# Kernel tuning notes

Measured on AMD Instinct MI355X. Metric: run time of the kernel, lower is better.

## Reference

```python
import jax, jax.numpy as jnp
import numpy as np
from jax import lax

IC, OC, K = 512, 512, 3
EPS = 1e-8
BLUR = np.array([1.0, 3.0, 3.0, 1.0], dtype=np.float32)


def setup_inputs() -> dict:
    key = jax.random.key(0)
    k1, k2 = jax.random.split(key)
    x = jax.random.normal(k1, (1, IC, 128, 128), dtype=jnp.float32)
    weight = jax.random.normal(k2, (1, OC, IC, K, K), dtype=jnp.float32)
    return {"x": x, "weight": weight}


def _blur_kernel():
    k1d = BLUR / BLUR.sum()  # normalize before outer product is equiv (sum of outer = 1)
    k2d = np.outer(k1d, k1d)
    k2d = k2d / k2d.sum()
    k2d = k2d * 4.0  # upsample_factor ** 2
    return jnp.asarray(k2d, dtype=jnp.float32)


def reference(x, weight):
    # x: (1, IC, H, W); weight: (1, OC, IC, K, K)
    scale = 1.0 / np.sqrt(IC * K * K)
    w = scale * weight
    # demodulation (batch = 1)
    demod = lax.rsqrt(jnp.sum(w * w, axis=(2, 3, 4)) + EPS)  # (1, OC)
    w = w * demod[:, :, None, None, None]
    w = w[0]  # (OC, IC, K, K)

    # conv_transpose2d(stride=2, padding=0) == conv with lhs_dilation=2,
    # spatial pad K-1, and spatially-flipped kernel.
    wt = jnp.flip(w, axis=(2, 3))  # (OC, IC, K, K)
    out = lax.conv_general_dilated(
        x, wt,
        window_strides=(1, 1),
        padding=[(K - 1, K - 1), (K - 1, K - 1)],
        lhs_dilation=(2, 2),
        dimension_numbers=("NCHW", "OIHW", "NCHW"),
    )  # (1, OC, 2H+1, 2W+1) = (1, 512, 257, 257)

    # Blur: depthwise FIR filter, pad0 = pad1 = 1, kernel 4x4 (upfirdn2d flips kernel)
    bk = jnp.flip(_blur_kernel(), axis=(0, 1))  # (4, 4), symmetric so flip is a no-op
    bkern = jnp.broadcast_to(bk[None, None], (OC, 1, 4, 4))
    out = lax.conv_general_dilated(
        out, bkern,
        window_strides=(1, 1),
        padding=[(1, 1), (1, 1)],
        feature_group_count=OC,
        dimension_numbers=("NCHW", "OIHW", "NCHW"),
    )  # (1, OC, 256, 256)
    return out
```

## Files before the change

### kernel.cpp

```cpp
#include <hip/hip_runtime.h>
#include <hip/hip_bf16.h>

#define ICN 512
#define OCN 512
#define RS    136
#define NROW  17792
#define GUARD 144
#define XROWS 17936

typedef __attribute__((ext_vector_type(8))) short short8;
typedef __attribute__((ext_vector_type(4))) float f32x4;

__device__ __forceinline__ void gload_lds16(const void* g, void* l) {
  __builtin_amdgcn_global_load_lds(
      (const __attribute__((address_space(1))) void*)g,
      (__attribute__((address_space(3))) void*)l, 16, 0, 0);
}

__global__ __launch_bounds__(256) void wprep_k(const float* __restrict__ w,
                                               __hip_bfloat16* __restrict__ AP) {
  constexpr int WIDX[9] = {0, 2, 6, 8, 1, 7, 3, 5, 4};
  const int oc = blockIdx.x;
  const int tid = threadIdx.x, lane = tid & 63, wv = tid >> 6;

  float v[2][9];
  float s = 0.f;
#pragma unroll
  for (int rep = 0; rep < 2; ++rep) {
    const int ic = tid + rep * 256;
    const float* wp = w + ((size_t)oc * ICN + ic) * 9;
#pragma unroll
    for (int j = 0; j < 9; ++j) { v[rep][j] = wp[j]; s += wp[j] * wp[j]; }
  }
#pragma unroll
  for (int o = 32; o > 0; o >>= 1) s += __shfl_down(s, o, 64);
  __shared__ float red[4];
  if (lane == 0) red[wv] = s;
  __syncthreads();
  const float tot = red[0] + red[1] + red[2] + red[3];
  const float scale2 = 1.0f / 4608.0f;
  const float c = sqrtf(scale2) * rsqrtf(scale2 * tot + 1e-8f);

#pragma unroll
  for (int rep = 0; rep < 2; ++rep) {
    const int ic = tid + rep * 256;
#pragma unroll
    for (int tp = 0; tp < 9; ++tp)
      AP[((size_t)tp * OCN + oc) * ICN + ic] = __float2bfloat16(c * v[rep][WIDX[tp]]);
  }
}

__global__ __launch_bounds__(256) void packx2_k(const float* __restrict__ x,
                                                unsigned int* __restrict__ XP32) {
  const int py  = blockIdx.x;
  const int ic0 = blockIdx.y * 64;
  const int tid = threadIdx.x;
  const int yy  = py - 1;
  const bool rowvalid = (unsigned)yy < 128u;

  __shared__ __hip_bfloat16 T[128 * 65];

  if (rowvalid) {
    const float4* xr = (const float4*)(x + (size_t)ic0 * 16384 + (size_t)yy * 128);
#pragma unroll
    for (int rep = 0; rep < 8; ++rep) {
      const int idx = rep * 256 + tid;
      const int x4 = idx & 31, ici = idx >> 5;
      const float4 v = xr[(size_t)ici * 4096 + x4];
      const int xx = x4 * 4;
      T[(xx + 0) * 65 + ici] = __float2bfloat16(v.x);
      T[(xx + 1) * 65 + ici] = __float2bfloat16(v.y);
      T[(xx + 2) * 65 + ici] = __float2bfloat16(v.z);
      T[(xx + 3) * 65 + ici] = __float2bfloat16(v.w);
    }
  }
  __syncthreads();

  const size_t rowbase = (size_t)(GUARD + py * 136) * 256 + (ic0 >> 1);
  for (int rep = 0; rep < 17; ++rep) {
    const int idx = rep * 256 + tid;
    const int px = idx >> 5, j = idx & 31;
    unsigned int uv = 0;
    if (rowvalid && (unsigned)(px - 1) < 128u) {
      union { __hip_bfloat16 h[2]; unsigned int u; } cv;
      cv.h[0] = T[(px - 1) * 65 + 2 * j];
      cv.h[1] = T[(px - 1) * 65 + 2 * j + 1];
      uv = cv.u;
    }
    XP32[rowbase + (size_t)px * 256 + j] = uv;
  }
}

__global__ __launch_bounds__(256) void zguard_k(unsigned int* __restrict__ XP32) {
  const int r = blockIdx.x;
  const int row = (r < 144) ? r : (r + 17680);
  XP32[(size_t)row * 256 + threadIdx.x] = 0;
}

__global__ __launch_bounds__(256) void gemm_k(const __hip_bfloat16* __restrict__ AP,
                                              const __hip_bfloat16* __restrict__ XPT,
                                              __hip_bfloat16* __restrict__ C) {
  constexpr int NTt[4]   = {4, 2, 2, 1};
  constexpr int TPO[4]   = {0, 4, 6, 8};
  constexpr int SHIFT[9] = {0, 1, 136, 137, 0, 136, 0, 1, 0};
  constexpr int AR[4]    = {129, 129, 128, 128};
  constexpr int AC[4]    = {129, 128, 129, 128};

  const int n0 = blockIdx.x * 128, oc0 = blockIdx.y * 128, ph = blockIdx.z;
  const int tid = threadIdx.x, lane = tid & 63, wv = tid >> 6;
  const int wr = wv >> 1, wc = wv & 1;

  __shared__ __align__(16) __hip_bfloat16 lA[128 * 32];
  __shared__ __align__(16) __hip_bfloat16 lB[128 * 32];

  const int srow = tid >> 2;
  const int scol = (tid & 3) * 8;
  __hip_bfloat16* ldA0 = &lA[wv * 512];
  __hip_bfloat16* ldA1 = &lA[wv * 512 + 2048];
  __hip_bfloat16* ldB0 = &lB[wv * 512];
  __hip_bfloat16* ldB1 = &lB[wv * 512 + 2048];

  f32x4 acc[4][4];
#pragma unroll
  for (int m = 0; m < 4; ++m)
#pragma unroll
    for (int n = 0; n < 4; ++n) acc[m][n] = (f32x4){0.f, 0.f, 0.f, 0.f};

  const int ntaps = NTt[ph];
  for (int t = 0; t < ntaps; ++t) {
    const int tp = TPO[ph] + t;
    const __hip_bfloat16* Ab = AP + (size_t)tp * (ICN * OCN) + (size_t)oc0 * ICN;
    const __hip_bfloat16* Bb = XPT + (size_t)(GUARD + n0 - SHIFT[tp]) * ICN;
    for (int ks = 0; ks < 16; ++ks) {
      const int kc = ks * 32 + scol;
      gload_lds16(Ab + (size_t)srow * ICN + kc, ldA0);
      gload_lds16(Ab + (size_t)(srow + 64) * ICN + kc, ldA1);
      gload_lds16(Bb + (size_t)srow * ICN + kc, ldB0);
      gload_lds16(Bb + (size_t)(srow + 64) * ICN + kc, ldB1);
      __syncthreads();
      short8 af[4], bfr[4];
#pragma unroll
      for (int m = 0; m < 4; ++m)
        af[m] = *(const short8*)&lA[(wr * 64 + m * 16 + (lane & 15)) * 32 + (lane >> 4) * 8];
#pragma unroll
      for (int n = 0; n < 4; ++n)
        bfr[n] = *(const short8*)&lB[(wc * 64 + n * 16 + (lane & 15)) * 32 + (lane >> 4) * 8];
#pragma unroll
      for (int m = 0; m < 4; ++m)
#pragma unroll
        for (int n = 0; n < 4; ++n)
          acc[m][n] = __builtin_amdgcn_mfma_f32_16x16x32_bf16(af[m], bfr[n], acc[m][n], 0, 0, 0);
      __syncthreads();
    }
  }

  const int lr = (lane >> 4) * 4, lc = lane & 15;
#pragma unroll
  for (int n = 0; n < 4; ++n) {
    const int col = n0 + wc * 64 + n * 16 + lc;
    const int pa = col / 136, pb = col - pa * 136;
    const bool ok = ((unsigned)(pa - 1) < (unsigned)AR[ph]) &&
                    ((unsigned)(pb - 1) < (unsigned)AC[ph]);
#pragma unroll
    for (int m = 0; m < 4; ++m)
#pragma unroll
      for (int r = 0; r < 4; ++r) {
        const int row = oc0 + wr * 64 + m * 16 + lr + r;
        C[((size_t)(ph * OCN + row)) * NROW + col] =
            __float2bfloat16(ok ? acc[m][n][r] : 0.f);
      }
  }
}

struct __align__(8) U4 { unsigned int w[4]; };

__global__ __launch_bounds__(256) void blur2_k(const unsigned short* __restrict__ C,
                                               float* __restrict__ out) {
  const int tid = threadIdx.x;
  const int t  = tid & 31;
  const int m  = blockIdx.x * 8 + (tid >> 5);
  const int oc = blockIdx.y;
  const float cfv[4] = {0.25f, 0.75f, 0.75f, 0.25f};

  float acc[8];
#pragma unroll
  for (int s = 0; s < 8; ++s) acc[s] = 0.f;

#pragma unroll
  for (int i = 0; i < 4; ++i) {
    const int u  = m - 1 + i;
    const int py = u & 1;
    const int r  = (u >> 1) + 1;
    const size_t base = (size_t)r * 136 + 4 * t;
    const U4 ev = *(const U4*)(C + ((size_t)(py * 2 + 0) * OCN + oc) * NROW + base);
    const U4 ov = *(const U4*)(C + ((size_t)(py * 2 + 1) * OCN + oc) * NROW + base);
    float E[8], O[8];
#pragma unroll
    for (int j = 0; j < 4; ++j) {
      E[2 * j]     = __uint_as_float(ev.w[j] << 16);
      E[2 * j + 1] = __uint_as_float(ev.w[j] & 0xffff0000u);
      O[2 * j]     = __uint_as_float(ov.w[j] << 16);
      O[2 * j + 1] = __uint_as_float(ov.w[j] & 0xffff0000u);
    }
    const float cv = cfv[i];
#pragma unroll
    for (int s = 0; s < 8; ++s) {
      float h;
      if ((s & 1) == 0) {
        const int k = s >> 1;
        h = 0.75f * E[k + 1] + 0.25f * E[k + 2] + 0.25f * O[k] + 0.75f * O[k + 1];
      } else {
        const int k = (s + 1) >> 1;
        h = 0.25f * E[k] + 0.75f * E[k + 1] + 0.75f * O[k] + 0.25f * O[k + 1];
      }
      acc[s] += cv * h;
    }
  }

  float* op = out + ((size_t)oc * 256 + m) * 256 + 8 * t;
  f32x4 s0 = {acc[0], acc[1], acc[2], acc[3]};
  f32x4 s1 = {acc[4], acc[5], acc[6], acc[7]};
  *(f32x4*)op = s0;
  *(f32x4*)(op + 4) = s1;
}

extern "C" void kernel_launch(void* const* d_in, const int* in_sizes, int n_in,
                              void* d_out, int out_size, void* d_ws, size_t ws_size,
                              hipStream_t stream) {
  const float* x = (const float*)d_in[0];
  const float* w = (const float*)d_in[1];
  float* out = (float*)d_out;

  __hip_bfloat16* AP  = (__hip_bfloat16*)d_ws;
  __hip_bfloat16* XPT = (__hip_bfloat16*)((char*)d_ws + 4718592);
  __hip_bfloat16* C   = (__hip_bfloat16*)((char*)d_ws + 23085056);

  wprep_k<<<512, 256, 0, stream>>>(w, AP);
  zguard_k<<<256, 256, 0, stream>>>((unsigned int*)XPT);
  packx2_k<<<dim3(130, 8), 256, 0, stream>>>(x, (unsigned int*)XPT);
  gemm_k<<<dim3(NROW / 128, 4, 4), 256, 0, stream>>>(AP, XPT, C);
  blur2_k<<<dim3(32, 512), 256, 0, stream>>>((const unsigned short*)C, out);
}
```

Baseline: 173.1 us.

## Restructure GEMM to 256x256 tiles with triple-buffered swizzled LDS pipeline

Enlarges the GEMM block tile to 256x256 with 512 threads and BK=32 bf16 (64 bytes). It adds a 3-stage LDS ring filled asynchronously via global_load_lds, with an XOR swizzle to avoid bank conflicts and explicit waitcnt, raw barriers and setprio to overlap loads with MFMA. This targets the per-k-step full synchronisation and low reuse of the 128x128 single-buffered version. In exchange it brings a much larger register and LDS footprint, far fewer blocks (560 vs 1112), and an out-of-bounds column guard since 256 does not divide NROW.

```diff
diff --git a/kernel.cpp b/kernel.cpp
--- a/kernel.cpp
+++ b/kernel.cpp
@@ -15,6 +15,12 @@
   __builtin_amdgcn_global_load_lds(
       (const __attribute__((address_space(1))) void*)g,
       (__attribute__((address_space(3))) void*)l, 16, 0, 0);
+}
+
+__device__ __forceinline__ void bar_raw() {
+  asm volatile("" ::: "memory");
+  __builtin_amdgcn_s_barrier();
+  asm volatile("" ::: "memory");
 }
 
 __global__ __launch_bounds__(256) void wprep_k(const float* __restrict__ w,
@@ -97,78 +103,113 @@
   XP32[(size_t)row * 256 + threadIdx.x] = 0;
 }
 
-__global__ __launch_bounds__(256) void gemm_k(const __hip_bfloat16* __restrict__ AP,
-                                              const __hip_bfloat16* __restrict__ XPT,
-                                              __hip_bfloat16* __restrict__ C) {
+__global__ __launch_bounds__(512, 2) void gemm_k(const __hip_bfloat16* __restrict__ AP,
+                                                 const __hip_bfloat16* __restrict__ XPT,
+                                                 __hip_bfloat16* __restrict__ C) {
   constexpr int NTt[4]   = {4, 2, 2, 1};
   constexpr int TPO[4]   = {0, 4, 6, 8};
   constexpr int SHIFT[9] = {0, 1, 136, 137, 0, 136, 0, 1, 0};
   constexpr int AR[4]    = {129, 129, 128, 128};
   constexpr int AC[4]    = {129, 128, 129, 128};
 
-  const int n0 = blockIdx.x * 128, oc0 = blockIdx.y * 128, ph = blockIdx.z;
+  const int n0 = blockIdx.x * 256, oc0 = blockIdx.y * 256, ph = blockIdx.z;
   const int tid = threadIdx.x, lane = tid & 63, wv = tid >> 6;
-  const int wr = wv >> 1, wc = wv & 1;
-
-  __shared__ __align__(16) __hip_bfloat16 lA[128 * 32];
-  __shared__ __align__(16) __hip_bfloat16 lB[128 * 32];
-
-  const int srow = tid >> 2;
-  const int scol = (tid & 3) * 8;
-  __hip_bfloat16* ldA0 = &lA[wv * 512];
-  __hip_bfloat16* ldA1 = &lA[wv * 512 + 2048];
-  __hip_bfloat16* ldB0 = &lB[wv * 512];
-  __hip_bfloat16* ldB1 = &lB[wv * 512 + 2048];
-
-  f32x4 acc[4][4];
-#pragma unroll
-  for (int m = 0; m < 4; ++m)
+  const int wr = wv >> 2, wc = wv & 3;
+  const int klane = (lane >> 4) * 16;
+
+  __shared__ __align__(16) char lds[3 * 32768];
+
+  const int T = NTt[ph] * 16;
+
+  auto STAGE = [&](int ts, int buf) {
+    const int tp = TPO[ph] + (ts >> 4);
+    const size_t kt64 = (size_t)(ts & 15) * 64;
+    const char* Ab = (const char*)AP + (size_t)tp * (512 * 1024) +
+                     (size_t)oc0 * 1024 + kt64;
+    const char* Bb = (const char*)XPT +
+                     (size_t)(GUARD + n0 - SHIFT[tp]) * 1024 + kt64;
+    char* L = lds + buf * 32768;
+#pragma unroll
+    for (int o = 0; o < 2; ++o) {
+      const int d = o * 8192 + tid * 16;
+      const int s = d ^ (((d >> 6) & 3) << 4);
+      gload_lds16(Ab + (s >> 6) * 1024 + (s & 63), L + o * 8192 + wv * 1024);
+    }
+#pragma unroll
+    for (int o = 0; o < 2; ++o) {
+      const int d = o * 8192 + tid * 16;
+      const int s = d ^ (((d >> 6) & 3) << 4);
+      gload_lds16(Bb + (s >> 6) * 1024 + (s & 63),
+                  L + 16384 + o * 8192 + wv * 1024);
+    }
+  };
+
+  f32x4 acc[8][4];
+#pragma unroll
+  for (int m = 0; m < 8; ++m)
 #pragma unroll
     for (int n = 0; n < 4; ++n) acc[m][n] = (f32x4){0.f, 0.f, 0.f, 0.f};
 
-  const int ntaps = NTt[ph];
-  for (int t = 0; t < ntaps; ++t) {
-    const int tp = TPO[ph] + t;
-    const __hip_bfloat16* Ab = AP + (size_t)tp * (ICN * OCN) + (size_t)oc0 * ICN;
-    const __hip_bfloat16* Bb = XPT + (size_t)(GUARD + n0 - SHIFT[tp]) * ICN;
-    for (int ks = 0; ks < 16; ++ks) {
-      const int kc = ks * 32 + scol;
-      gload_lds16(Ab + (size_t)srow * ICN + kc, ldA0);
-      gload_lds16(Ab + (size_t)(srow + 64) * ICN + kc, ldA1);
-      gload_lds16(Bb + (size_t)srow * ICN + kc, ldB0);
-      gload_lds16(Bb + (size_t)(srow + 64) * ICN + kc, ldB1);
-      __syncthreads();
-      short8 af[4], bfr[4];
-#pragma unroll
-      for (int m = 0; m < 4; ++m)
-        af[m] = *(const short8*)&lA[(wr * 64 + m * 16 + (lane & 15)) * 32 + (lane >> 4) * 8];
+  STAGE(0, 0);
+  STAGE(1, 1);
+
+  for (int t = 0; t < T; ++t) {
+    const int ts = (t + 2 < T) ? (t + 2) : (T - 1);
+    STAGE(ts, (t + 2) % 3);
+    asm volatile("s_waitcnt vmcnt(8)" ::: "memory");
+    __builtin_amdgcn_sched_barrier(0);
+    bar_raw();
+
+    const char* LA = lds + (t % 3) * 32768;
+    const char* LB = LA + 16384;
+    short8 bf[4], af[8];
+#pragma unroll
+    for (int n = 0; n < 4; ++n) {
+      const int b = (wc * 64 + n * 16 + (lane & 15)) * 64 + klane;
+      bf[n] = *(const short8*)(LB + (b ^ (((b >> 6) & 3) << 4)));
+    }
+#pragma unroll
+    for (int m = 0; m < 8; ++m) {
+      const int a = (wr * 128 + m * 16 + (lane & 15)) * 64 + klane;
+      af[m] = *(const short8*)(LA + (a ^ (((a >> 6) & 3) << 4)));
+    }
+    asm volatile("s_waitcnt lgkmcnt(4)");
+    __builtin_amdgcn_sched_barrier(0);
+    __builtin_amdgcn_s_setprio(1);
+#pragma unroll
+    for (int m = 0; m < 4; ++m)
 #pragma unroll
       for (int n = 0; n < 4; ++n)
-        bfr[n] = *(const short8*)&lB[(wc * 64 + n * 16 + (lane & 15)) * 32 + (lane >> 4) * 8];
-#pragma unroll
-      for (int m = 0; m < 4; ++m)
-#pragma unroll
-        for (int n = 0; n < 4; ++n)
-          acc[m][n] = __builtin_amdgcn_mfma_f32_16x16x32_bf16(af[m], bfr[n], acc[m][n], 0, 0, 0);
-      __syncthreads();
-    }
+        acc[m][n] = __builtin_amdgcn_mfma_f32_16x16x32_bf16(af[m], bf[n], acc[m][n], 0, 0, 0);
+    asm volatile("s_waitcnt lgkmcnt(0)");
+    __builtin_amdgcn_sched_barrier(0);
+#pragma unroll
+    for (int m = 4; m < 8; ++m)
+#pragma unroll
+      for (int n = 0; n < 4; ++n)
+        acc[m][n] = __builtin_amdgcn_mfma_f32_16x16x32_bf16(af[m], bf[n], acc[m][n], 0, 0, 0);
+    __builtin_amdgcn_s_setprio(0);
+    asm volatile("s_waitcnt lgkmcnt(0)" ::: "memory");
+    bar_raw();
   }
 
   const int lr = (lane >> 4) * 4, lc = lane & 15;
 #pragma unroll
   for (int n = 0; n < 4; ++n) {
     const int col = n0 + wc * 64 + n * 16 + lc;
-    const int pa = col / 136, pb = col - pa * 136;
-    const bool ok = ((unsigned)(pa - 1) < (unsigned)AR[ph]) &&
-                    ((unsigned)(pb - 1) < (unsigned)AC[ph]);
-#pragma unroll
-    for (int m = 0; m < 4; ++m)
-#pragma unroll
-      for (int r = 0; r < 4; ++r) {
-        const int row = oc0 + wr * 64 + m * 16 + lr + r;
-        C[((size_t)(ph * OCN + row)) * NROW + col] =
-            __float2bfloat16(ok ? acc[m][n][r] : 0.f);
-      }
+    if (col < NROW) {
+      const int pa = col / 136, pb = col - pa * 136;
+      const bool ok = ((unsigned)(pa - 1) < (unsigned)AR[ph]) &&
+                      ((unsigned)(pb - 1) < (unsigned)AC[ph]);
+#pragma unroll
+      for (int m = 0; m < 8; ++m)
+#pragma unroll
+        for (int r = 0; r < 4; ++r) {
+          const int row = oc0 + wr * 128 + m * 16 + lr + r;
+          C[((size_t)(ph * OCN + row)) * NROW + col] =
+              __float2bfloat16(ok ? acc[m][n][r] : 0.f);
+        }
+    }
   }
 }
 
@@ -238,6 +279,6 @@
   wprep_k<<<512, 256, 0, stream>>>(w, AP);
   zguard_k<<<256, 256, 0, stream>>>((unsigned int*)XPT);
   packx2_k<<<dim3(130, 8), 256, 0, stream>>>(x, (unsigned int*)XPT);
-  gemm_k<<<dim3(NROW / 128, 4, 4), 256, 0, stream>>>(AP, XPT, C);
+  gemm_k<<<dim3(70, 2, 4), 512, 0, stream>>>(AP, XPT, C);
   blur2_k<<<dim3(32, 512), 256, 0, stream>>>((const unsigned short*)C, out);
 }
```

New measurement: 165.0 us. 4.7% less time.

## Restructure GEMM: fragment-ordered weights from global, double-buffered swizzled LDS for activations

Applied to the files above, without the earlier changes.

Weights are repacked into an MFMA-fragment-ordered layout so each lane loads its A fragments directly from global memory, bypassing LDS. Only the activation tile goes through LDS, now double-buffered across the K loop with an XOR swizzle and one barrier per 128-wide K step. The block grows to 512 threads covering a 128x256 output tile, with a bounds check on the last column tile and raised MFMA priority. The aim is to cut LDS traffic, barrier count and load latency, at the cost of more global A reads per block and higher register and LDS pressure.

```diff
diff --git a/kernel.cpp b/kernel.cpp
--- a/kernel.cpp
+++ b/kernel.cpp
@@ -17,8 +17,14 @@
       (__attribute__((address_space(3))) void*)l, 16, 0, 0);
 }
 
+__device__ __forceinline__ void bar_raw() {
+  asm volatile("" ::: "memory");
+  __builtin_amdgcn_s_barrier();
+  asm volatile("" ::: "memory");
+}
+
 __global__ __launch_bounds__(256) void wprep_k(const float* __restrict__ w,
-                                               __hip_bfloat16* __restrict__ AP) {
+                                               __hip_bfloat16* __restrict__ AF) {
   constexpr int WIDX[9] = {0, 2, 6, 8, 1, 7, 3, 5, 4};
   const int oc = blockIdx.x;
   const int tid = threadIdx.x, lane = tid & 63, wv = tid >> 6;
@@ -44,9 +50,12 @@
 #pragma unroll
   for (int rep = 0; rep < 2; ++rep) {
     const int ic = tid + rep * 256;
-#pragma unroll
-    for (int tp = 0; tp < 9; ++tp)
-      AP[((size_t)tp * OCN + oc) * ICN + ic] = __float2bfloat16(c * v[rep][WIDX[tp]]);
+    const size_t inr = (size_t)(((oc & 15) | (((ic >> 3) & 3) << 4)) * 8 + (ic & 7));
+#pragma unroll
+    for (int tp = 0; tp < 9; ++tp) {
+      const size_t rec = ((size_t)tp * 32 + (oc >> 4)) * 16 + (ic >> 5);
+      AF[rec * 512 + inr] = __float2bfloat16(c * v[rep][WIDX[tp]]);
+    }
   }
 }
 
@@ -97,28 +106,38 @@
   XP32[(size_t)row * 256 + threadIdx.x] = 0;
 }
 
-__global__ __launch_bounds__(256) void gemm_k(const __hip_bfloat16* __restrict__ AP,
-                                              const __hip_bfloat16* __restrict__ XPT,
-                                              __hip_bfloat16* __restrict__ C) {
+__global__ __launch_bounds__(512, 4) void gemm_k(const __hip_bfloat16* __restrict__ AF,
+                                                 const __hip_bfloat16* __restrict__ XPT,
+                                                 __hip_bfloat16* __restrict__ C) {
   constexpr int NTt[4]   = {4, 2, 2, 1};
   constexpr int TPO[4]   = {0, 4, 6, 8};
   constexpr int SHIFT[9] = {0, 1, 136, 137, 0, 136, 0, 1, 0};
   constexpr int AR[4]    = {129, 129, 128, 128};
   constexpr int AC[4]    = {129, 128, 129, 128};
 
-  const int n0 = blockIdx.x * 128, oc0 = blockIdx.y * 128, ph = blockIdx.z;
+  const int n0 = blockIdx.x * 256, oc0 = blockIdx.y * 128, ph = blockIdx.z;
   const int tid = threadIdx.x, lane = tid & 63, wv = tid >> 6;
-  const int wr = wv >> 1, wc = wv & 1;
-
-  __shared__ __align__(16) __hip_bfloat16 lA[128 * 32];
-  __shared__ __align__(16) __hip_bfloat16 lB[128 * 32];
-
-  const int srow = tid >> 2;
-  const int scol = (tid & 3) * 8;
-  __hip_bfloat16* ldA0 = &lA[wv * 512];
-  __hip_bfloat16* ldA1 = &lA[wv * 512 + 2048];
-  __hip_bfloat16* ldB0 = &lB[wv * 512];
-  __hip_bfloat16* ldB1 = &lB[wv * 512 + 2048];
+  const int wr = wv >> 2, wc = wv & 3;
+  const int lane15 = lane & 15, l7 = lane & 7;
+  const int kx = (lane >> 4) * 16;
+
+  __shared__ __align__(16) char lds[2 * 32768];
+
+  const int T = NTt[ph] * 8;
+
+  const int r0  = tid >> 3;
+  const int wk0 = ((tid * 16) & 127) ^ ((r0 & 7) << 4);
+
+  auto STG = [&](int i, char* Lb) {
+    const int tp = TPO[ph] + (i >> 3);
+    const size_t kb = (size_t)(i & 7) * 128;
+    const char* Bg = (const char*)XPT +
+                     (size_t)(GUARD + n0 - SHIFT[tp]) * 1024 + kb;
+#pragma unroll
+    for (int g = 0; g < 4; ++g)
+      gload_lds16(Bg + (size_t)(g * 64 + r0) * 1024 + wk0,
+                  Lb + g * 8192 + wv * 1024);
+  };
 
   f32x4 acc[4][4];
 #pragma unroll
@@ -126,49 +145,63 @@
 #pragma unroll
     for (int n = 0; n < 4; ++n) acc[m][n] = (f32x4){0.f, 0.f, 0.f, 0.f};
 
-  const int ntaps = NTt[ph];
-  for (int t = 0; t < ntaps; ++t) {
-    const int tp = TPO[ph] + t;
-    const __hip_bfloat16* Ab = AP + (size_t)tp * (ICN * OCN) + (size_t)oc0 * ICN;
-    const __hip_bfloat16* Bb = XPT + (size_t)(GUARD + n0 - SHIFT[tp]) * ICN;
-    for (int ks = 0; ks < 16; ++ks) {
-      const int kc = ks * 32 + scol;
-      gload_lds16(Ab + (size_t)srow * ICN + kc, ldA0);
-      gload_lds16(Ab + (size_t)(srow + 64) * ICN + kc, ldA1);
-      gload_lds16(Bb + (size_t)srow * ICN + kc, ldB0);
-      gload_lds16(Bb + (size_t)(srow + 64) * ICN + kc, ldB1);
-      __syncthreads();
-      short8 af[4], bfr[4];
+  STG(0, lds);
+  asm volatile("s_waitcnt vmcnt(0)" ::: "memory");
+  bar_raw();
+
+  for (int i = 0; i < T; ++i) {
+    const int buf = i & 1;
+    const char* LB = lds + buf * 32768;
+    char* Ln = lds + (buf ^ 1) * 32768;
+    const int ts = (i + 1 < T) ? (i + 1) : (T - 1);
+    STG(ts, Ln);
+
+    const int tp = TPO[ph] + (i >> 3);
+    const char* AFt = (const char*)AF +
+        ((size_t)((tp * 32 + (oc0 >> 4) + wr * 4) * 16 + (i & 7) * 2) << 10) +
+        (size_t)lane * 16;
+
+#pragma unroll
+    for (int kh = 0; kh < 2; ++kh) {
+      short8 bf[4], af[4];
+#pragma unroll
+      for (int n = 0; n < 4; ++n) {
+        const int e = (wc * 64 + n * 16 + lane15) * 128 + kh * 64 + kx;
+        bf[n] = *(const short8*)(LB + (e ^ (l7 << 4)));
+      }
 #pragma unroll
       for (int m = 0; m < 4; ++m)
-        af[m] = *(const short8*)&lA[(wr * 64 + m * 16 + (lane & 15)) * 32 + (lane >> 4) * 8];
-#pragma unroll
-      for (int n = 0; n < 4; ++n)
-        bfr[n] = *(const short8*)&lB[(wc * 64 + n * 16 + (lane & 15)) * 32 + (lane >> 4) * 8];
+        af[m] = *(const short8*)(AFt + ((size_t)(m * 16 + kh) << 10));
+      __builtin_amdgcn_s_setprio(1);
 #pragma unroll
       for (int m = 0; m < 4; ++m)
 #pragma unroll
         for (int n = 0; n < 4; ++n)
-          acc[m][n] = __builtin_amdgcn_mfma_f32_16x16x32_bf16(af[m], bfr[n], acc[m][n], 0, 0, 0);
-      __syncthreads();
-    }
+          acc[m][n] = __builtin_amdgcn_mfma_f32_16x16x32_bf16(af[m], bf[n], acc[m][n], 0, 0, 0);
+      __builtin_amdgcn_s_setprio(0);
+    }
+
+    asm volatile("s_waitcnt vmcnt(0)" ::: "memory");
+    bar_raw();
   }
 
   const int lr = (lane >> 4) * 4, lc = lane & 15;
 #pragma unroll
   for (int n = 0; n < 4; ++n) {
     const int col = n0 + wc * 64 + n * 16 + lc;
-    const int pa = col / 136, pb = col - pa * 136;
-    const bool ok = ((unsigned)(pa - 1) < (unsigned)AR[ph]) &&
-                    ((unsigned)(pb - 1) < (unsigned)AC[ph]);
-#pragma unroll
-    for (int m = 0; m < 4; ++m)
-#pragma unroll
-      for (int r = 0; r < 4; ++r) {
-        const int row = oc0 + wr * 64 + m * 16 + lr + r;
-        C[((size_t)(ph * OCN + row)) * NROW + col] =
-            __float2bfloat16(ok ? acc[m][n][r] : 0.f);
-      }
+    if (col < NROW) {
+      const int pa = col / 136, pb = col - pa * 136;
+      const bool ok = ((unsigned)(pa - 1) < (unsigned)AR[ph]) &&
+                      ((unsigned)(pb - 1) < (unsigned)AC[ph]);
+#pragma unroll
+      for (int m = 0; m < 4; ++m)
+#pragma unroll
+        for (int r = 0; r < 4; ++r) {
+          const int row = oc0 + wr * 64 + m * 16 + lr + r;
+          C[((size_t)(ph * OCN + row)) * NROW + col] =
+              __float2bfloat16(ok ? acc[m][n][r] : 0.f);
+        }
+    }
   }
 }
 
@@ -231,13 +264,13 @@
   const float* w = (const float*)d_in[1];
   float* out = (float*)d_out;
 
-  __hip_bfloat16* AP  = (__hip_bfloat16*)d_ws;
+  __hip_bfloat16* AF  = (__hip_bfloat16*)d_ws;
   __hip_bfloat16* XPT = (__hip_bfloat16*)((char*)d_ws + 4718592);
   __hip_bfloat16* C   = (__hip_bfloat16*)((char*)d_ws + 23085056);
 
-  wprep_k<<<512, 256, 0, stream>>>(w, AP);
+  wprep_k<<<512, 256, 0, stream>>>(w, AF);
   zguard_k<<<256, 256, 0, stream>>>((unsigned int*)XPT);
   packx2_k<<<dim3(130, 8), 256, 0, stream>>>(x, (unsigned int*)XPT);
-  gemm_k<<<dim3(NROW / 128, 4, 4), 256, 0, stream>>>(AP, XPT, C);
+  gemm_k<<<dim3(70, 4, 4), 512, 0, stream>>>(AF, XPT, C);
   blur2_k<<<dim3(32, 512), 256, 0, stream>>>((const unsigned short*)C, out);
 }
```

Measured after the change: 177.1 us. 2.3% more time.
